# Kernel optimization log

Hardware: AMD Instinct MI355X
Metric: run time of the kernel (lower is better)

## Reference

```python
import jax, jax.numpy as jnp
import numpy as np

HEADS = 16
DIM_HEAD = 64
SCALE = DIM_HEAD ** -0.5
NEG = -jnp.finfo(jnp.float32).max


def setup_inputs() -> dict:
    key = jax.random.key(0)
    k1, k2, k3, k4, k5 = jax.random.split(key, 5)
    dim = 1024
    inner = HEADS * DIM_HEAD
    b, n = 2, 2048
    s = dim ** -0.5
    return {
        "x": jax.random.normal(k1, (b, n, dim), dtype=jnp.float32),
        "Wq": jax.random.normal(k2, (dim, inner), dtype=jnp.float32) * s,
        "Wk": jax.random.normal(k3, (dim, inner), dtype=jnp.float32) * s,
        "Wv": jax.random.normal(k4, (dim, inner), dtype=jnp.float32) * s,
        "Wo": jax.random.normal(k5, (inner, dim), dtype=jnp.float32) * s,
    }


def reference(x, Wq, Wk, Wv, Wo):
    b, n, _ = x.shape
    # project and split heads: b n (h d) -> b h n d
    def split(t):
        return t.reshape(b, n, HEADS, DIM_HEAD).transpose(0, 2, 1, 3)
    q = split(x @ Wq) * SCALE
    k = split(x @ Wk)
    v = split(x @ Wv)
    sim = jnp.einsum('bhid,bhjd->bhij', q, k)
    # causal mask: triu(j - i + 1) masked with -finfo.max
    causal = jnp.triu(jnp.ones((n, n), dtype=bool), k=1)
    sim = jnp.where(causal, NEG, sim)
    attn = jax.nn.softmax(sim, axis=-1)  # dropout p=0.0 -> identity
    out = jnp.einsum('bhij,bhjd->bhid', attn, v)
    out = out.transpose(0, 2, 1, 3).reshape(b, n, HEADS * DIM_HEAD)
    return out @ Wo
```

## Files before the change

### kernel.cpp

```cpp
#include <hip/hip_runtime.h>

#define NHEAD 16
#define DHEAD 64
#define SEQ 2048
#define DMODEL 1024
#define BATCH 2
#define QSCALE 0.1803368801111204f

typedef __bf16 bf16x8 __attribute__((ext_vector_type(8)));
typedef float f32x4 __attribute__((ext_vector_type(4)));
typedef float f32x16 __attribute__((ext_vector_type(16)));
typedef unsigned int u32x4 __attribute__((ext_vector_type(4)));

__device__ inline unsigned short f2bf(float f) {
  unsigned int u = __builtin_bit_cast(unsigned int, f);
  u = (u + 0x7FFFu + ((u >> 16) & 1u)) >> 16;
  return (unsigned short)u;
}

__device__ inline unsigned int cvtpk_bf16(float lo, float hi) {
  unsigned int r;
  asm("v_cvt_pk_bf16_f32 %0, %1, %2" : "=v"(r) : "v"(lo), "v"(hi));
  return r;
}

__device__ inline void pl32swap(unsigned int& a, unsigned int& b) {
  asm volatile("v_permlane32_swap_b32 %0, %1" : "+v"(a), "+v"(b));
}

typedef __attribute__((address_space(1))) unsigned int GU32;
typedef __attribute__((address_space(3))) unsigned int LU32;
__device__ inline void gld_lds16(const void* g, void* l) {
  __builtin_amdgcn_global_load_lds((GU32*)g, (LU32*)l, 16, 0, 0);
}

__global__ __launch_bounds__(256) void k_conv_x(const float* __restrict__ x,
                                                unsigned short* __restrict__ Af) {
  int blk = blockIdx.x;
  int R = blk >> 5, kt = blk & 31;
  int t = threadIdx.x;
  int i = t >> 6, lane = t & 63;
  int n = R * 64 + i * 16 + (lane & 15);
  int k = kt * 32 + (lane >> 4) * 8;
  const float* xp = x + (size_t)n * DMODEL + k;
  float4 v0 = *(const float4*)xp;
  float4 v1 = *(const float4*)(xp + 4);
  ushort4 lo, hi;
  lo.x = f2bf(v0.x); lo.y = f2bf(v0.y); lo.z = f2bf(v0.z); lo.w = f2bf(v0.w);
  hi.x = f2bf(v1.x); hi.y = f2bf(v1.y); hi.z = f2bf(v1.z); hi.w = f2bf(v1.w);
  size_t base = ((size_t)((R * 32 + kt) * 4 + i) * 64 + lane) * 8;
  *(ushort4*)&Af[base] = lo;
  *(ushort4*)&Af[base + 4] = hi;
}

__global__ __launch_bounds__(256) void k_trans_wf(const float* __restrict__ Wq, const float* __restrict__ Wk,
                                                  const float* __restrict__ Wv,
                                                  unsigned short* __restrict__ Wqf, unsigned short* __restrict__ Wkf,
                                                  unsigned short* __restrict__ Wvf) {
  __shared__ float ts[32][65];
  int mat = blockIdx.z;
  const float* src = (mat == 0) ? Wq : (mat == 1) ? Wk : Wv;
  unsigned short* dst = (mat == 0) ? Wqf : (mat == 1) ? Wkf : Wvf;
  int cb = blockIdx.x, kt = blockIdx.y;
  int t = threadIdx.x;
  int row = t >> 3, seg = t & 7;
  const float* sp = src + (size_t)(kt * 32 + row) * DMODEL + cb * 64 + seg * 8;
  float4 u0 = *(const float4*)sp;
  float4 u1 = *(const float4*)(sp + 4);
  ts[row][seg * 8 + 0] = u0.x; ts[row][seg * 8 + 1] = u0.y;
  ts[row][seg * 8 + 2] = u0.z; ts[row][seg * 8 + 3] = u0.w;
  ts[row][seg * 8 + 4] = u1.x; ts[row][seg * 8 + 5] = u1.y;
  ts[row][seg * 8 + 6] = u1.z; ts[row][seg * 8 + 7] = u1.w;
  __syncthreads();
  int j = t >> 6, lane = t & 63;
  int c_l = j * 16 + (lane & 15);
  int kb = (lane >> 4) * 8;
  ushort4 lo, hi;
  lo.x = f2bf(ts[kb + 0][c_l]); lo.y = f2bf(ts[kb + 1][c_l]);
  lo.z = f2bf(ts[kb + 2][c_l]); lo.w = f2bf(ts[kb + 3][c_l]);
  hi.x = f2bf(ts[kb + 4][c_l]); hi.y = f2bf(ts[kb + 5][c_l]);
  hi.z = f2bf(ts[kb + 6][c_l]); hi.w = f2bf(ts[kb + 7][c_l]);
  size_t base = ((size_t)((cb * 32 + kt) * 4 + j) * 64 + lane) * 8;
  *(ushort4*)&dst[base] = lo;
  *(ushort4*)&dst[base + 4] = hi;
}

__global__ __launch_bounds__(256) void k_trans_wo(const float* __restrict__ Wo,
                                                  unsigned short* __restrict__ Wot) {
  __shared__ float ts[64][65];
  int r0 = blockIdx.y * 64, c0 = blockIdx.x * 64;
  int t = threadIdx.x;
  int tr = t >> 4, tc = (t & 15) * 4;
#pragma unroll
  for (int i = 0; i < 4; i++) {
    int row = tr + i * 16;
    float4 v = *(const float4*)&Wo[(size_t)(r0 + row) * DMODEL + c0 + tc];
    ts[row][tc + 0] = v.x; ts[row][tc + 1] = v.y; ts[row][tc + 2] = v.z; ts[row][tc + 3] = v.w;
  }
  __syncthreads();
#pragma unroll
  for (int i = 0; i < 4; i++) {
    int nrow = tr + i * 16;
    ushort4 o;
    o.x = f2bf(ts[tc + 0][nrow]); o.y = f2bf(ts[tc + 1][nrow]);
    o.z = f2bf(ts[tc + 2][nrow]); o.w = f2bf(ts[tc + 3][nrow]);
    *(ushort4*)&Wot[(size_t)(c0 + nrow) * DMODEL + r0 + tc] = o;
  }
}

__global__ __launch_bounds__(64, 2) void k_gemm_qkv(const unsigned short* __restrict__ Af,
                                                    const unsigned short* __restrict__ Wqf,
                                                    const unsigned short* __restrict__ Wkf,
                                                    const unsigned short* __restrict__ Wvf,
                                                    unsigned short* __restrict__ Qf,
                                                    unsigned short* __restrict__ Kf,
                                                    unsigned short* __restrict__ Vf) {
  int id = blockIdx.x;
  int xcd = id & 7, lid = id >> 3;
  int rw = lid / 12, cw = lid % 12;
  int R = (xcd >> 1) * 16 + rw;
  int ct = (xcd & 1) * 12 + cw;
  int mat = ct >> 3, cb2 = ct & 7;
  const unsigned short* Bf = (mat == 0) ? Wqf : (mat == 1) ? Wkf : Wvf;
  int lane = threadIdx.x;
  const unsigned short* Ap  = Af + (size_t)R * 65536 + lane * 8;
  const unsigned short* Bp0 = Bf + (size_t)(cb2 * 2) * 65536 + lane * 8;
  const unsigned short* Bp1 = Bp0 + 65536;

  f32x4 acc[4][8] = {};
  bf16x8 a0[4], a1[4], b0[8], b1[8];
#pragma unroll
  for (int i = 0; i < 4; i++) a0[i] = *(const bf16x8*)(Ap + i * 512);
#pragma unroll
  for (int j = 0; j < 4; j++) {
    b0[j]     = *(const bf16x8*)(Bp0 + j * 512);
    b0[4 + j] = *(const bf16x8*)(Bp1 + j * 512);
  }
#pragma unroll 1
  for (int kt = 0; kt < 32; kt += 2) {
    {
      const unsigned short* An = Ap + (kt + 1) * 2048;
      const unsigned short* Bn0 = Bp0 + (kt + 1) * 2048;
      const unsigned short* Bn1 = Bp1 + (kt + 1) * 2048;
#pragma unroll
      for (int i = 0; i < 4; i++) a1[i] = *(const bf16x8*)(An + i * 512);
#pragma unroll
      for (int j = 0; j < 4; j++) {
        b1[j]     = *(const bf16x8*)(Bn0 + j * 512);
        b1[4 + j] = *(const bf16x8*)(Bn1 + j * 512);
      }
    }
#pragma unroll
    for (int i = 0; i < 4; i++)
#pragma unroll
      for (int j = 0; j < 8; j++)
        acc[i][j] = __builtin_amdgcn_mfma_f32_16x16x32_bf16(a0[i], b0[j], acc[i][j], 0, 0, 0);
    if (kt + 2 < 32) {
      const unsigned short* An = Ap + (kt + 2) * 2048;
      const unsigned short* Bn0 = Bp0 + (kt + 2) * 2048;
      const unsigned short* Bn1 = Bp1 + (kt + 2) * 2048;
#pragma unroll
      for (int i = 0; i < 4; i++) a0[i] = *(const bf16x8*)(An + i * 512);
#pragma unroll
      for (int j = 0; j < 4; j++) {
        b0[j]     = *(const bf16x8*)(Bn0 + j * 512);
        b0[4 + j] = *(const bf16x8*)(Bn1 + j * 512);
      }
    }
#pragma unroll
    for (int i = 0; i < 4; i++)
#pragma unroll
      for (int j = 0; j < 8; j++)
        acc[i][j] = __builtin_amdgcn_mfma_f32_16x16x32_bf16(a1[i], b1[j], acc[i][j], 0, 0, 0);
  }

#pragma unroll
  for (int i = 0; i < 4; i++)
#pragma unroll
    for (int j = 0; j < 8; j++) {
      int n_g = R * 64 + i * 16 + ((lane >> 4) << 2);
      int c = cb2 * 128 + j * 16 + (lane & 15);
      int b = n_g >> 11, n0 = n_g & 2047;
      int h = c >> 6, d = c & 63;
      int bh = b * NHEAD + h;
      if (mat == 0) {
        size_t base = ((size_t)(bh * 64 + (n0 >> 5)) * 4 + (d >> 4)) * 512 +
                      (size_t)((((d >> 3) & 1) * 32 + (n0 & 31)) * 8 + (d & 7));
#pragma unroll
        for (int r = 0; r < 4; r++) Qf[base + 8 * r] = f2bf(acc[i][j][r] * QSCALE);
      } else if (mat == 1) {
        size_t base = ((size_t)(bh * 32 + (n0 >> 6)) * 8 + ((d >> 4) + 4 * ((n0 >> 5) & 1))) * 512 +
                      (size_t)((((d >> 3) & 1) * 32 + (n0 & 31)) * 8 + (d & 7));
#pragma unroll
        for (int r = 0; r < 4; r++) Kf[base + 8 * r] = f2bf(acc[i][j][r]);
      } else {
        size_t base = ((size_t)(bh * 32 + (n0 >> 6)) * 8 + (((n0 >> 4) & 3) + 4 * (d >> 5))) * 512 +
                      (size_t)((((n0 >> 3) & 1) * 32 + (d & 31)) * 8 + (n0 & 7));
        ushort4 o;
        o.x = f2bf(acc[i][j][0]); o.y = f2bf(acc[i][j][1]);
        o.z = f2bf(acc[i][j][2]); o.w = f2bf(acc[i][j][3]);
        *(ushort4*)&Vf[base] = o;
      }
    }
}

__device__ inline void gemm_core(const unsigned short* __restrict__ A, const unsigned short* __restrict__ Bt,
                                 int brow0, int bcol0, unsigned short* As, unsigned short* Bs,
                                 f32x4 acc[4][4]) {
  int tid = threadIdx.x, lane = tid & 63, wave = tid >> 6;
  int wr = wave >> 1, wc = wave & 1;
  for (int kt = 0; kt < DMODEL / 32; ++kt) {
    int k0 = kt * 32;
    if (kt) __syncthreads();
#pragma unroll
    for (int qi = 0; qi < 2; ++qi) {
      int e0 = (wave * 2 + qi) * 512;
      int e = e0 + lane * 8;
      gld_lds16(&A[(size_t)(brow0 + (e >> 5)) * DMODEL + k0 + (e & 31)], &As[e0]);
      gld_lds16(&Bt[(size_t)(bcol0 + (e >> 5)) * DMODEL + k0 + (e & 31)], &Bs[e0]);
    }
    __syncthreads();
    bf16x8 af[4], bff[4];
#pragma unroll
    for (int i = 0; i < 4; i++)
      af[i] = *(const bf16x8*)&As[(wr * 64 + i * 16 + (lane & 15)) * 32 + (lane >> 4) * 8];
#pragma unroll
    for (int j = 0; j < 4; j++)
      bff[j] = *(const bf16x8*)&Bs[(wc * 64 + j * 16 + (lane & 15)) * 32 + (lane >> 4) * 8];
#pragma unroll
    for (int i = 0; i < 4; i++)
#pragma unroll
      for (int j = 0; j < 4; j++)
        acc[i][j] = __builtin_amdgcn_mfma_f32_16x16x32_bf16(af[i], bff[j], acc[i][j], 0, 0, 0);
  }
}

__global__ __launch_bounds__(64, 2) void k_attn(const unsigned short* __restrict__ Qf,
                                                const unsigned short* __restrict__ Kf,
                                                const unsigned short* __restrict__ Vf,
                                                unsigned short* __restrict__ Ob) {
  int id = blockIdx.x;
  int xcd = id & 7, m = id >> 3;
  int bhl = m & 3, u = m >> 2;
  int bh = xcd * 4 + bhl;
  int v = (u < 32) ? (63 - u) : (u - 32);
  int nk = (v >> 1) + 1;
  int lane = threadIdx.x;
  int h = lane >> 5, ql = lane & 31;
  int qrow = v * 32 + ql;

  const unsigned short* Qp = Qf + (size_t)bh * 131072 + (size_t)v * 2048;
  const unsigned short* Kp = Kf + (size_t)bh * 131072;
  const unsigned short* Vp = Vf + (size_t)bh * 131072;
  int b = bh >> 4, hh = bh & 15;

  bf16x8 qv[4];
#pragma unroll
  for (int ds = 0; ds < 4; ds++)
    qv[ds] = *(const bf16x8*)&Qp[ds * 512 + lane * 8];

  bf16x8 Kr[8], Vr[8];
#pragma unroll
  for (int jj = 0; jj < 8; jj++) Kr[jj] = *(const bf16x8*)&Kp[jj * 512 + lane * 8];
#pragma unroll
  for (int jj = 0; jj < 8; jj++) Vr[jj] = *(const bf16x8*)&Vp[jj * 512 + lane * 8];

  f32x16 o0 = {}, o1 = {};
  float m_r = -3.0e38f, l_r = 0.0f;

#pragma unroll 1
  for (int kc = 0; kc < nk; ++kc) {
    f32x16 s0 = {}, s1 = {};
#pragma unroll
    for (int ds = 0; ds < 4; ds++) {
      s0 = __builtin_amdgcn_mfma_f32_32x32x16_bf16(Kr[ds], qv[ds], s0, 0, 0, 0);
      s1 = __builtin_amdgcn_mfma_f32_32x32x16_bf16(Kr[4 + ds], qv[ds], s1, 0, 0, 0);
    }
    bool pfn = (kc + 1 < nk);
    size_t nb = (size_t)(kc + 1) * 4096;
    if (pfn) {
#pragma unroll
      for (int jj = 0; jj < 8; jj++) Kr[jj] = *(const bf16x8*)&Kp[nb + jj * 512 + lane * 8];
    }
    int k0 = kc * 64;
    if (kc == nk - 1) {
#pragma unroll
      for (int r = 0; r < 16; r++) {
        int kloc = (r & 3) + 8 * (r >> 2) + 4 * h;
        if (k0 + kloc > qrow) s0[r] = -3.0e38f;
        if (k0 + 32 + kloc > qrow) s1[r] = -3.0e38f;
      }
    }
    float t0[8], t1[8];
#pragma unroll
    for (int r = 0; r < 8; r++) t0[r] = fmaxf(s0[r], s0[r + 8]);
#pragma unroll
    for (int r = 0; r < 8; r++) t1[r] = fmaxf(s1[r], s1[r + 8]);
#pragma unroll
    for (int r = 0; r < 4; r++) t0[r] = fmaxf(fmaxf(t0[r], t0[r + 4]), fmaxf(t1[r], t1[r + 4]));
    float pm = fmaxf(fmaxf(t0[0], t0[1]), fmaxf(t0[2], t0[3]));
    pm = fmaxf(pm, __shfl_xor(pm, 32));
    bool grow = pm > m_r + 8.0f;
    float mnew = grow ? pm : m_r;
    float sf = grow ? __builtin_amdgcn_exp2f(m_r - mnew) : 1.0f;
    m_r = mnew;
    float rsum = 0.0f;
#pragma unroll
    for (int r = 0; r < 16; r++) { s0[r] = __builtin_amdgcn_exp2f(s0[r] - m_r); rsum += s0[r]; }
#pragma unroll
    for (int r = 0; r < 16; r++) { s1[r] = __builtin_amdgcn_exp2f(s1[r] - m_r); rsum += s1[r]; }
    l_r = l_r * sf + rsum;
    if (__ballot(grow)) {
#pragma unroll
      for (int r = 0; r < 16; r++) { o0[r] *= sf; o1[r] *= sf; }
    }
    unsigned int pa0 = cvtpk_bf16(s0[0], s0[1]),   pa1 = cvtpk_bf16(s0[2], s0[3]);
    unsigned int pb0 = cvtpk_bf16(s0[4], s0[5]),   pb1 = cvtpk_bf16(s0[6], s0[7]);
    unsigned int pc0 = cvtpk_bf16(s0[8], s0[9]),   pc1 = cvtpk_bf16(s0[10], s0[11]);
    unsigned int pd0 = cvtpk_bf16(s0[12], s0[13]), pd1 = cvtpk_bf16(s0[14], s0[15]);
    unsigned int pe0 = cvtpk_bf16(s1[0], s1[1]),   pe1 = cvtpk_bf16(s1[2], s1[3]);
    unsigned int pf0 = cvtpk_bf16(s1[4], s1[5]),   pf1 = cvtpk_bf16(s1[6], s1[7]);
    unsigned int pg0 = cvtpk_bf16(s1[8], s1[9]),   pg1 = cvtpk_bf16(s1[10], s1[11]);
    unsigned int ph0 = cvtpk_bf16(s1[12], s1[13]), ph1 = cvtpk_bf16(s1[14], s1[15]);
    pl32swap(pa0, pb0); pl32swap(pa1, pb1);
    pl32swap(pc0, pd0); pl32swap(pc1, pd1);
    pl32swap(pe0, pf0); pl32swap(pe1, pf1);
    pl32swap(pg0, ph0); pl32swap(pg1, ph1);
    bf16x8 pfr[4];
    pfr[0] = __builtin_bit_cast(bf16x8, (u32x4){pa0, pa1, pb0, pb1});
    pfr[1] = __builtin_bit_cast(bf16x8, (u32x4){pc0, pc1, pd0, pd1});
    pfr[2] = __builtin_bit_cast(bf16x8, (u32x4){pe0, pe1, pf0, pf1});
    pfr[3] = __builtin_bit_cast(bf16x8, (u32x4){pg0, pg1, ph0, ph1});
#pragma unroll
    for (int ks = 0; ks < 4; ks++) {
      o0 = __builtin_amdgcn_mfma_f32_32x32x16_bf16(Vr[ks], pfr[ks], o0, 0, 0, 0);
      o1 = __builtin_amdgcn_mfma_f32_32x32x16_bf16(Vr[4 + ks], pfr[ks], o1, 0, 0, 0);
    }
    if (pfn) {
#pragma unroll
      for (int jj = 0; jj < 8; jj++) Vr[jj] = *(const bf16x8*)&Vp[nb + jj * 512 + lane * 8];
    }
  }

  float lt = l_r + __shfl_xor(l_r, 32);
  float rl = 1.0f / lt;
  size_t obase = ((size_t)(b * SEQ + qrow)) * DMODEL + hh * DHEAD;
#pragma unroll
  for (int rg = 0; rg < 4; rg++) {
    uint2 w0, w1;
    w0.x = cvtpk_bf16(o0[4 * rg] * rl, o0[4 * rg + 1] * rl);
    w0.y = cvtpk_bf16(o0[4 * rg + 2] * rl, o0[4 * rg + 3] * rl);
    w1.x = cvtpk_bf16(o1[4 * rg] * rl, o1[4 * rg + 1] * rl);
    w1.y = cvtpk_bf16(o1[4 * rg + 2] * rl, o1[4 * rg + 3] * rl);
    *(uint2*)&Ob[obase + 8 * rg + 4 * h] = w0;
    *(uint2*)&Ob[obase + 32 + 8 * rg + 4 * h] = w1;
  }
}

__global__ __launch_bounds__(256) void k_gemm_out(const unsigned short* __restrict__ Ob,
                                                  const unsigned short* __restrict__ Wot,
                                                  float* __restrict__ out) {
  __shared__ unsigned short As[128 * 32];
  __shared__ unsigned short Bs[128 * 32];
  int col0 = blockIdx.x * 128;
  int brow0 = blockIdx.y * 128;
  int lane = threadIdx.x & 63, wave = threadIdx.x >> 6;
  int wr = wave >> 1, wc = wave & 1;
  f32x4 acc[4][4] = {};
  gemm_core(Ob, Wot, brow0, col0, As, Bs, acc);
#pragma unroll
  for (int i = 0; i < 4; i++)
#pragma unroll
    for (int j = 0; j < 4; j++)
#pragma unroll
      for (int r = 0; r < 4; r++) {
        int row = brow0 + wr * 64 + i * 16 + ((lane >> 4) << 2) + r;
        int c = col0 + wc * 64 + j * 16 + (lane & 15);
        out[(size_t)row * DMODEL + c] = acc[i][j][r];
      }
}

extern "C" void kernel_launch(void* const* d_in, const int* in_sizes, int n_in,
                              void* d_out, int out_size, void* d_ws, size_t ws_size,
                              hipStream_t stream) {
  const float* x  = (const float*)d_in[0];
  const float* Wq = (const float*)d_in[1];
  const float* Wk = (const float*)d_in[2];
  const float* Wv = (const float*)d_in[3];
  const float* Wo = (const float*)d_in[4];
  float* out = (float*)d_out;
  char* ws = (char*)d_ws;
  unsigned short* Af  = (unsigned short*)(ws);
  unsigned short* Wqf = (unsigned short*)(ws + (8ull << 20));
  unsigned short* Wkf = (unsigned short*)(ws + (10ull << 20));
  unsigned short* Wvf = (unsigned short*)(ws + (12ull << 20));
  unsigned short* Wot = (unsigned short*)(ws + (14ull << 20));
  unsigned short* Qf  = (unsigned short*)(ws + (16ull << 20));
  unsigned short* Kf  = (unsigned short*)(ws + (24ull << 20));
  unsigned short* Vf  = (unsigned short*)(ws + (32ull << 20));
  unsigned short* Ob  = (unsigned short*)(ws + (40ull << 20));

  k_conv_x<<<dim3(2048), dim3(256), 0, stream>>>(x, Af);
  k_trans_wf<<<dim3(16, 32, 3), dim3(256), 0, stream>>>(Wq, Wk, Wv, Wqf, Wkf, Wvf);
  k_trans_wo<<<dim3(16, 16), dim3(256), 0, stream>>>(Wo, Wot);
  k_gemm_qkv<<<dim3(1536), dim3(64), 0, stream>>>(Af, Wqf, Wkf, Wvf, Qf, Kf, Vf);
  k_attn<<<dim3(2048), dim3(64), 0, stream>>>(Qf, Kf, Vf, Ob);
  k_gemm_out<<<dim3(8, 32), dim3(256), 0, stream>>>(Ob, Wot, out);
}
```

Measured before the change: 106.9 us.

## Write attention output in fragment layout and use register-direct output GEMM

The attention kernel now stores its output directly in the pre-swizzled MFMA fragment layout, and Wo is converted by the shared weight-transform kernel. This removes the separate Wo transpose launch. The output projection drops the LDS-staged gemm_core and instead streams fragments straight from global memory into registers with double buffering, one wave per 64x64 tile. The QKV GEMM is regrouped to two waves per block. Together these aim to cut a launch, LDS traffic and block-level syncs, at the cost of lower per-block reuse and more global fragment loads.

```diff
diff --git a/kernel.cpp b/kernel.cpp
--- a/kernel.cpp
+++ b/kernel.cpp
@@ -26,12 +26,6 @@
 
 __device__ inline void pl32swap(unsigned int& a, unsigned int& b) {
   asm volatile("v_permlane32_swap_b32 %0, %1" : "+v"(a), "+v"(b));
-}
-
-typedef __attribute__((address_space(1))) unsigned int GU32;
-typedef __attribute__((address_space(3))) unsigned int LU32;
-__device__ inline void gld_lds16(const void* g, void* l) {
-  __builtin_amdgcn_global_load_lds((GU32*)g, (LU32*)l, 16, 0, 0);
 }
 
 __global__ __launch_bounds__(256) void k_conv_x(const float* __restrict__ x,
@@ -54,13 +48,13 @@
 }
 
 __global__ __launch_bounds__(256) void k_trans_wf(const float* __restrict__ Wq, const float* __restrict__ Wk,
-                                                  const float* __restrict__ Wv,
+                                                  const float* __restrict__ Wv, const float* __restrict__ Wo,
                                                   unsigned short* __restrict__ Wqf, unsigned short* __restrict__ Wkf,
-                                                  unsigned short* __restrict__ Wvf) {
+                                                  unsigned short* __restrict__ Wvf, unsigned short* __restrict__ Wof) {
   __shared__ float ts[32][65];
   int mat = blockIdx.z;
-  const float* src = (mat == 0) ? Wq : (mat == 1) ? Wk : Wv;
-  unsigned short* dst = (mat == 0) ? Wqf : (mat == 1) ? Wkf : Wvf;
+  const float* src = (mat == 0) ? Wq : (mat == 1) ? Wk : (mat == 2) ? Wv : Wo;
+  unsigned short* dst = (mat == 0) ? Wqf : (mat == 1) ? Wkf : (mat == 2) ? Wvf : Wof;
   int cb = blockIdx.x, kt = blockIdx.y;
   int t = threadIdx.x;
   int row = t >> 3, seg = t & 7;
@@ -85,44 +79,23 @@
   *(ushort4*)&dst[base + 4] = hi;
 }
 
-__global__ __launch_bounds__(256) void k_trans_wo(const float* __restrict__ Wo,
-                                                  unsigned short* __restrict__ Wot) {
-  __shared__ float ts[64][65];
-  int r0 = blockIdx.y * 64, c0 = blockIdx.x * 64;
-  int t = threadIdx.x;
-  int tr = t >> 4, tc = (t & 15) * 4;
-#pragma unroll
-  for (int i = 0; i < 4; i++) {
-    int row = tr + i * 16;
-    float4 v = *(const float4*)&Wo[(size_t)(r0 + row) * DMODEL + c0 + tc];
-    ts[row][tc + 0] = v.x; ts[row][tc + 1] = v.y; ts[row][tc + 2] = v.z; ts[row][tc + 3] = v.w;
-  }
-  __syncthreads();
-#pragma unroll
-  for (int i = 0; i < 4; i++) {
-    int nrow = tr + i * 16;
-    ushort4 o;
-    o.x = f2bf(ts[tc + 0][nrow]); o.y = f2bf(ts[tc + 1][nrow]);
-    o.z = f2bf(ts[tc + 2][nrow]); o.w = f2bf(ts[tc + 3][nrow]);
-    *(ushort4*)&Wot[(size_t)(c0 + nrow) * DMODEL + r0 + tc] = o;
-  }
-}
-
-__global__ __launch_bounds__(64, 2) void k_gemm_qkv(const unsigned short* __restrict__ Af,
-                                                    const unsigned short* __restrict__ Wqf,
-                                                    const unsigned short* __restrict__ Wkf,
-                                                    const unsigned short* __restrict__ Wvf,
-                                                    unsigned short* __restrict__ Qf,
-                                                    unsigned short* __restrict__ Kf,
-                                                    unsigned short* __restrict__ Vf) {
+__global__ __launch_bounds__(128, 2) void k_gemm_qkv(const unsigned short* __restrict__ Af,
+                                                     const unsigned short* __restrict__ Wqf,
+                                                     const unsigned short* __restrict__ Wkf,
+                                                     const unsigned short* __restrict__ Wvf,
+                                                     unsigned short* __restrict__ Qf,
+                                                     unsigned short* __restrict__ Kf,
+                                                     unsigned short* __restrict__ Vf) {
   int id = blockIdx.x;
   int xcd = id & 7, lid = id >> 3;
-  int rw = lid / 12, cw = lid % 12;
-  int R = (xcd >> 1) * 16 + rw;
+  int rq = lid / 12, cw = lid % 12;
+  int rho = (xcd >> 1) * 8 + rq;
+  int wv = threadIdx.x >> 6;
+  int R = rho * 2 + wv;
   int ct = (xcd & 1) * 12 + cw;
   int mat = ct >> 3, cb2 = ct & 7;
   const unsigned short* Bf = (mat == 0) ? Wqf : (mat == 1) ? Wkf : Wvf;
-  int lane = threadIdx.x;
+  int lane = threadIdx.x & 63;
   const unsigned short* Ap  = Af + (size_t)R * 65536 + lane * 8;
   const unsigned short* Bp0 = Bf + (size_t)(cb2 * 2) * 65536 + lane * 8;
   const unsigned short* Bp1 = Bp0 + 65536;
@@ -204,41 +177,10 @@
     }
 }
 
-__device__ inline void gemm_core(const unsigned short* __restrict__ A, const unsigned short* __restrict__ Bt,
-                                 int brow0, int bcol0, unsigned short* As, unsigned short* Bs,
-                                 f32x4 acc[4][4]) {
-  int tid = threadIdx.x, lane = tid & 63, wave = tid >> 6;
-  int wr = wave >> 1, wc = wave & 1;
-  for (int kt = 0; kt < DMODEL / 32; ++kt) {
-    int k0 = kt * 32;
-    if (kt) __syncthreads();
-#pragma unroll
-    for (int qi = 0; qi < 2; ++qi) {
-      int e0 = (wave * 2 + qi) * 512;
-      int e = e0 + lane * 8;
-      gld_lds16(&A[(size_t)(brow0 + (e >> 5)) * DMODEL + k0 + (e & 31)], &As[e0]);
-      gld_lds16(&Bt[(size_t)(bcol0 + (e >> 5)) * DMODEL + k0 + (e & 31)], &Bs[e0]);
-    }
-    __syncthreads();
-    bf16x8 af[4], bff[4];
-#pragma unroll
-    for (int i = 0; i < 4; i++)
-      af[i] = *(const bf16x8*)&As[(wr * 64 + i * 16 + (lane & 15)) * 32 + (lane >> 4) * 8];
-#pragma unroll
-    for (int j = 0; j < 4; j++)
-      bff[j] = *(const bf16x8*)&Bs[(wc * 64 + j * 16 + (lane & 15)) * 32 + (lane >> 4) * 8];
-#pragma unroll
-    for (int i = 0; i < 4; i++)
-#pragma unroll
-      for (int j = 0; j < 4; j++)
-        acc[i][j] = __builtin_amdgcn_mfma_f32_16x16x32_bf16(af[i], bff[j], acc[i][j], 0, 0, 0);
-  }
-}
-
 __global__ __launch_bounds__(64, 2) void k_attn(const unsigned short* __restrict__ Qf,
                                                 const unsigned short* __restrict__ Kf,
                                                 const unsigned short* __restrict__ Vf,
-                                                unsigned short* __restrict__ Ob) {
+                                                unsigned short* __restrict__ Obf) {
   int id = blockIdx.x;
   int xcd = id & 7, m = id >> 3;
   int bhl = m & 3, u = m >> 2;
@@ -344,7 +286,10 @@
 
   float lt = l_r + __shfl_xor(l_r, 32);
   float rl = 1.0f / lt;
-  size_t obase = ((size_t)(b * SEQ + qrow)) * DMODEL + hh * DHEAD;
+  int Rg = b * 32 + (v >> 1);
+  int ii = (v * 2 + (ql >> 4)) & 3;
+  size_t base0 = ((size_t)(Rg * 32 + 2 * hh) * 4 + ii) * 512 + (size_t)((ql & 15) * 8 + 4 * h);
+  size_t base1 = base0 + 2048;
 #pragma unroll
   for (int rg = 0; rg < 4; rg++) {
     uint2 w0, w1;
@@ -352,32 +297,71 @@
     w0.y = cvtpk_bf16(o0[4 * rg + 2] * rl, o0[4 * rg + 3] * rl);
     w1.x = cvtpk_bf16(o1[4 * rg] * rl, o1[4 * rg + 1] * rl);
     w1.y = cvtpk_bf16(o1[4 * rg + 2] * rl, o1[4 * rg + 3] * rl);
-    *(uint2*)&Ob[obase + 8 * rg + 4 * h] = w0;
-    *(uint2*)&Ob[obase + 32 + 8 * rg + 4 * h] = w1;
-  }
-}
-
-__global__ __launch_bounds__(256) void k_gemm_out(const unsigned short* __restrict__ Ob,
-                                                  const unsigned short* __restrict__ Wot,
-                                                  float* __restrict__ out) {
-  __shared__ unsigned short As[128 * 32];
-  __shared__ unsigned short Bs[128 * 32];
-  int col0 = blockIdx.x * 128;
-  int brow0 = blockIdx.y * 128;
-  int lane = threadIdx.x & 63, wave = threadIdx.x >> 6;
-  int wr = wave >> 1, wc = wave & 1;
+    *(uint2*)&Obf[base0 + rg * 128] = w0;
+    *(uint2*)&Obf[base1 + rg * 128] = w1;
+  }
+}
+
+__global__ __launch_bounds__(64, 2) void k_gemm_out(const unsigned short* __restrict__ Obf,
+                                                    const unsigned short* __restrict__ Wof,
+                                                    float* __restrict__ out) {
+  int id = blockIdx.x;
+  int xcd = id & 7, lid = id >> 3;
+  int rg8 = lid >> 4, cb = lid & 15;
+  int R = xcd * 8 + rg8;
+  int lane = threadIdx.x;
+  const unsigned short* Ap = Obf + (size_t)R * 65536 + lane * 8;
+  const unsigned short* Bp = Wof + (size_t)cb * 65536 + lane * 8;
+
   f32x4 acc[4][4] = {};
-  gemm_core(Ob, Wot, brow0, col0, As, Bs, acc);
+  bf16x8 a0[4], b0[4], a1[4], b1[4];
+#pragma unroll
+  for (int i = 0; i < 4; i++) {
+    a0[i] = *(const bf16x8*)(Ap + i * 512);
+    b0[i] = *(const bf16x8*)(Bp + i * 512);
+  }
+#pragma unroll 1
+  for (int kt = 0; kt < 32; kt += 2) {
+    {
+      const unsigned short* An = Ap + (kt + 1) * 2048;
+      const unsigned short* Bn = Bp + (kt + 1) * 2048;
+#pragma unroll
+      for (int i = 0; i < 4; i++) {
+        a1[i] = *(const bf16x8*)(An + i * 512);
+        b1[i] = *(const bf16x8*)(Bn + i * 512);
+      }
+    }
+#pragma unroll
+    for (int i = 0; i < 4; i++)
+#pragma unroll
+      for (int j = 0; j < 4; j++)
+        acc[i][j] = __builtin_amdgcn_mfma_f32_16x16x32_bf16(a0[i], b0[j], acc[i][j], 0, 0, 0);
+    if (kt + 2 < 32) {
+      const unsigned short* An = Ap + (kt + 2) * 2048;
+      const unsigned short* Bn = Bp + (kt + 2) * 2048;
+#pragma unroll
+      for (int i = 0; i < 4; i++) {
+        a0[i] = *(const bf16x8*)(An + i * 512);
+        b0[i] = *(const bf16x8*)(Bn + i * 512);
+      }
+    }
+#pragma unroll
+    for (int i = 0; i < 4; i++)
+#pragma unroll
+      for (int j = 0; j < 4; j++)
+        acc[i][j] = __builtin_amdgcn_mfma_f32_16x16x32_bf16(a1[i], b1[j], acc[i][j], 0, 0, 0);
+  }
+
 #pragma unroll
   for (int i = 0; i < 4; i++)
 #pragma unroll
-    for (int j = 0; j < 4; j++)
-#pragma unroll
-      for (int r = 0; r < 4; r++) {
-        int row = brow0 + wr * 64 + i * 16 + ((lane >> 4) << 2) + r;
-        int c = col0 + wc * 64 + j * 16 + (lane & 15);
-        out[(size_t)row * DMODEL + c] = acc[i][j][r];
-      }
+    for (int j = 0; j < 4; j++) {
+      int n_g = R * 64 + i * 16 + ((lane >> 4) << 2);
+      int c = cb * 64 + j * 16 + (lane & 15);
+#pragma unroll
+      for (int r = 0; r < 4; r++)
+        out[(size_t)(n_g + r) * DMODEL + c] = acc[i][j][r];
+    }
 }
 
 extern "C" void kernel_launch(void* const* d_in, const int* in_sizes, int n_in,
@@ -394,16 +378,15 @@
   unsigned short* Wqf = (unsigned short*)(ws + (8ull << 20));
   unsigned short* Wkf = (unsigned short*)(ws + (10ull << 20));
   unsigned short* Wvf = (unsigned short*)(ws + (12ull << 20));
-  unsigned short* Wot = (unsigned short*)(ws + (14ull << 20));
+  unsigned short* Wof = (unsigned short*)(ws + (14ull << 20));
   unsigned short* Qf  = (unsigned short*)(ws + (16ull << 20));
   unsigned short* Kf  = (unsigned short*)(ws + (24ull << 20));
   unsigned short* Vf  = (unsigned short*)(ws + (32ull << 20));
-  unsigned short* Ob  = (unsigned short*)(ws + (40ull << 20));
+  unsigned short* Obf = (unsigned short*)(ws + (40ull << 20));
 
   k_conv_x<<<dim3(2048), dim3(256), 0, stream>>>(x, Af);
-  k_trans_wf<<<dim3(16, 32, 3), dim3(256), 0, stream>>>(Wq, Wk, Wv, Wqf, Wkf, Wvf);
-  k_trans_wo<<<dim3(16, 16), dim3(256), 0, stream>>>(Wo, Wot);
-  k_gemm_qkv<<<dim3(1536), dim3(64), 0, stream>>>(Af, Wqf, Wkf, Wvf, Qf, Kf, Vf);
-  k_attn<<<dim3(2048), dim3(64), 0, stream>>>(Qf, Kf, Vf, Ob);
-  k_gemm_out<<<dim3(8, 32), dim3(256), 0, stream>>>(Ob, Wot, out);
-}
+  k_trans_wf<<<dim3(16, 32, 4), dim3(256), 0, stream>>>(Wq, Wk, Wv, Wo, Wqf, Wkf, Wvf, Wof);
+  k_gemm_qkv<<<dim3(768), dim3(128), 0, stream>>>(Af, Wqf, Wkf, Wvf, Qf, Kf, Vf);
+  k_attn<<<dim3(2048), dim3(64), 0, stream>>>(Qf, Kf, Vf, Obf);
+  k_gemm_out<<<dim3(1024), dim3(64), 0, stream>>>(Obf, Wof, out);
+}
```

Measured after the change: 109.8 us. +2.8%, slower.
